# Optimization experiments

Hardware: AMD Instinct MI355X
Metric: run time of the kernel (lower is better)

The kernel has to match this reference:

```python
import jax, jax.numpy as jnp
import numpy as np

BATCH = 8
HEADS = 16
Q_LEN = 1024
K_LEN = 1024
HEAD_DIM = 64


def setup_inputs() -> dict:
    key = jax.random.key(0)
    kq, kk, kv, kl = jax.random.split(key, 4)
    queries = jax.random.normal(kq, (BATCH * HEADS, Q_LEN, HEAD_DIM), dtype=jnp.float32)
    keys = jax.random.normal(kk, (BATCH * HEADS, K_LEN, HEAD_DIM), dtype=jnp.float32)
    values = jax.random.normal(kv, (BATCH * HEADS, K_LEN, HEAD_DIM), dtype=jnp.float32)
    valid_lens = jax.random.randint(kl, (BATCH,), 0, K_LEN, dtype=jnp.int64)
    return {"queries": queries, "keys": keys, "values": values, "valid_lens": valid_lens}


def reference(queries, keys, values, valid_lens):
    # queries/keys/values: [B*H, S, d]; valid_lens: [B] int
    bh, q_len, d = queries.shape
    k_len = keys.shape[1]
    b = valid_lens.shape[0]
    h = bh // b
    scale = 1.0 / float(d) ** 0.5
    # [B*H, q, k] scores
    scores = jnp.einsum("bqd,bkd->bqk", queries, keys) * scale
    # encode_mask: True where key position >= valid_len -> fill with -1e6
    mask = jnp.arange(k_len)[None, :] >= valid_lens[:, None]  # [B, k]
    scores = scores.reshape(b, h, q_len, k_len)
    scores = jnp.where(mask[:, None, None, :], jnp.float32(-1000000.0), scores)
    attn = jax.nn.softmax(scores, axis=-1)  # [B, H, q, k]
    out = jnp.einsum("bhqk,bhkd->bhqd", attn, values.reshape(b, h, k_len, d))
    return out.reshape(bh, q_len, d)
```

## Files before the change

### kernel.cpp

```cpp
#include <hip/hip_runtime.h>


#define H_PER_B 16
#define QL 1024
#define KL 1024
#define DH 64
#define KT 64
#define QW 16
#define NW 8
#define QB (QW * NW)
#define KST 72
#define VST 72
#define PST 72

typedef float  f32x4  __attribute__((ext_vector_type(4)));
typedef short  bf16x8 __attribute__((ext_vector_type(8)));
typedef short  bf16x4 __attribute__((ext_vector_type(4)));

__device__ __forceinline__ short f2bf(float f) {
    unsigned u = __builtin_bit_cast(unsigned, f);
    u += 0x7FFFu + ((u >> 16) & 1u);
    return (short)(u >> 16);
}

__global__ __launch_bounds__(512) void attn_fwd(
    const float* __restrict__ Q, const float* __restrict__ K,
    const float* __restrict__ V, const int* __restrict__ vlen_p,
    float* __restrict__ O)
{
    const int qtile = blockIdx.x;
    const int bh    = blockIdx.y;
    const int vlen  = vlen_p[bh / H_PER_B];

    const int tid  = threadIdx.x;
    const int wave = tid >> 6;
    const int lane = tid & 63;
    const int lg   = lane >> 4;
    const int lr   = lane & 15;

    const float* Qb = Q + ((size_t)bh * QL + (size_t)qtile * QB + (size_t)wave * QW) * DH;
    const float* Kb = K + (size_t)bh * KL * DH;
    const float* Vb = V + (size_t)bh * KL * DH;

    __shared__ short Ks[KT][KST];
    __shared__ short VsT[DH][VST];
    __shared__ short Ps[NW][QW][PST];

    bf16x8 qf[2];
#pragma unroll
    for (int dc = 0; dc < 2; ++dc) {
        const float* p = Qb + (size_t)lr * DH + dc * 32 + 8 * lg;
        float4 a = *(const float4*)p;
        float4 b = *(const float4*)(p + 4);
        bf16x8 t;
        t[0]=f2bf(a.x); t[1]=f2bf(a.y); t[2]=f2bf(a.z); t[3]=f2bf(a.w);
        t[4]=f2bf(b.x); t[5]=f2bf(b.y); t[6]=f2bf(b.z); t[7]=f2bf(b.w);
        qf[dc] = t;
    }

    f32x4 acc[4];
#pragma unroll
    for (int i = 0; i < 4; ++i) acc[i] = (f32x4){0.f, 0.f, 0.f, 0.f};
    float lsum[4] = {0.f, 0.f, 0.f, 0.f};

    const bool all_masked = (vlen == 0);

    const int vd  = tid & 63;
    const int vk0 = (tid >> 6) * 8;
    const float* Vcol = Vb + vd;

    for (int kt0 = 0; kt0 < KL; kt0 += KT) {
        __syncthreads();

#pragma unroll
        for (int i = 0; i < 2; ++i) {
            int idx = tid + i * 512;
            int kr  = idx >> 4;
            int dc0 = (idx & 15) * 4;
            float4 kv = *(const float4*)(Kb + (size_t)(kt0 + kr) * DH + dc0);
            bf16x4 t;
            t[0]=f2bf(kv.x); t[1]=f2bf(kv.y); t[2]=f2bf(kv.z); t[3]=f2bf(kv.w);
            *(bf16x4*)&Ks[kr][dc0] = t;
        }

        {
            float v[8];
#pragma unroll
            for (int j = 0; j < 8; ++j)
                v[j] = Vcol[(size_t)(kt0 + vk0 + j) * DH];
            bf16x8 t;
#pragma unroll
            for (int j = 0; j < 8; ++j) t[j] = f2bf(v[j]);
            *(bf16x8*)&VsT[vd][vk0] = t;
        }
        __syncthreads();

        f32x4 s[4];
#pragma unroll
        for (int kh = 0; kh < 4; ++kh) {
            f32x4 c = (f32x4){0.f, 0.f, 0.f, 0.f};
#pragma unroll
            for (int dc = 0; dc < 2; ++dc) {
                bf16x8 kf = *(const bf16x8*)&Ks[kh * 16 + lr][dc * 32 + 8 * lg];
                c = __builtin_amdgcn_mfma_f32_16x16x32_bf16(qf[dc], kf, c, 0, 0, 0);
            }
            s[kh] = c;
        }

#pragma unroll
        for (int kh = 0; kh < 4; ++kh) {
            const int  kpos   = kt0 + kh * 16 + lr;
            const bool masked = (kpos >= vlen);
#pragma unroll
            for (int r = 0; r < 4; ++r) {
                float p;
                if (masked) p = all_masked ? 1.0f : 0.0f;
                else        p = __expf(s[kh][r] * 0.125f);
                lsum[r] += p;
                Ps[wave][lg * 4 + r][kh * 16 + lr] = f2bf(p);
            }
        }

#pragma unroll
        for (int u = 0; u < 2; ++u) {
            bf16x8 pf = *(const bf16x8*)&Ps[wave][lr][u * 32 + 8 * lg];
#pragma unroll
            for (int dt = 0; dt < 4; ++dt) {
                bf16x8 vf = *(const bf16x8*)&VsT[dt * 16 + lr][u * 32 + 8 * lg];
                acc[dt] = __builtin_amdgcn_mfma_f32_16x16x32_bf16(pf, vf, acc[dt], 0, 0, 0);
            }
        }
    }

    float inv[4];
#pragma unroll
    for (int r = 0; r < 4; ++r) {
        float sum = lsum[r];
#pragma unroll
        for (int off = 1; off < 16; off <<= 1)
            sum += __shfl_xor(sum, off, 64);
        inv[r] = 1.0f / sum;
    }

    float* Ob = O + ((size_t)bh * QL + (size_t)qtile * QB + (size_t)wave * QW) * DH;
#pragma unroll
    for (int r = 0; r < 4; ++r)
#pragma unroll
        for (int dt = 0; dt < 4; ++dt)
            Ob[(size_t)(lg * 4 + r) * DH + dt * 16 + lr] = acc[dt][r] * inv[r];
}

extern "C" void kernel_launch(void* const* d_in, const int* in_sizes, int n_in,
                              void* d_out, int out_size, void* d_ws, size_t ws_size,
                              hipStream_t stream) {
    (void)in_sizes; (void)n_in; (void)d_ws; (void)ws_size; (void)out_size;
    const float* Q    = (const float*)d_in[0];
    const float* K    = (const float*)d_in[1];
    const float* V    = (const float*)d_in[2];
    const int*   vlen = (const int*)d_in[3];
    float*       O    = (float*)d_out;

    dim3 grid(QL / QB, 128);
    dim3 block(512);
    attn_fwd<<<grid, block, 0, stream>>>(Q, K, V, vlen, O);
}
```

Baseline: 194.2 us.

## Skip fully masked key tiles and double-buffer K/V staging

```diff
diff --git a/kernel.cpp b/kernel.cpp
--- a/kernel.cpp
+++ b/kernel.cpp
@@ -11,16 +11,22 @@
 #define QB (QW * NW)
 #define KST 72
 #define VST 72
-#define PST 72
+#define PST 68
 
 typedef float  f32x4  __attribute__((ext_vector_type(4)));
 typedef short  bf16x8 __attribute__((ext_vector_type(8)));
 typedef short  bf16x4 __attribute__((ext_vector_type(4)));
 
-__device__ __forceinline__ short f2bf(float f) {
+__device__ __forceinline__ unsigned bfbits(float f) {
     unsigned u = __builtin_bit_cast(unsigned, f);
     u += 0x7FFFu + ((u >> 16) & 1u);
-    return (short)(u >> 16);
+    return u >> 16;
+}
+__device__ __forceinline__ unsigned pk2(float a, float b) {
+    return bfbits(a) | (bfbits(b) << 16);
+}
+__device__ __forceinline__ short s2bf(float f) {
+    return (short)bfbits(f);
 }
 
 __global__ __launch_bounds__(512) void attn_fwd(
@@ -28,8 +34,8 @@
     const float* __restrict__ V, const int* __restrict__ vlen_p,
     float* __restrict__ O)
 {
-    const int qtile = blockIdx.x;
-    const int bh    = blockIdx.y;
+    const int bh    = blockIdx.x;
+    const int qtile = blockIdx.y;
     const int vlen  = vlen_p[bh / H_PER_B];
 
     const int tid  = threadIdx.x;
@@ -42,20 +48,23 @@
     const float* Kb = K + (size_t)bh * KL * DH;
     const float* Vb = V + (size_t)bh * KL * DH;
 
-    __shared__ short Ks[KT][KST];
-    __shared__ short VsT[DH][VST];
-    __shared__ short Ps[NW][QW][PST];
+    __shared__ short Ks [2][KT][KST];
+    __shared__ short VsT[2][DH][VST];
+    __shared__ short Ps [NW][QW][PST];
 
+    const float QSCALE = 0.18033688011112042f;
     bf16x8 qf[2];
 #pragma unroll
     for (int dc = 0; dc < 2; ++dc) {
         const float* p = Qb + (size_t)lr * DH + dc * 32 + 8 * lg;
         float4 a = *(const float4*)p;
         float4 b = *(const float4*)(p + 4);
-        bf16x8 t;
-        t[0]=f2bf(a.x); t[1]=f2bf(a.y); t[2]=f2bf(a.z); t[3]=f2bf(a.w);
-        t[4]=f2bf(b.x); t[5]=f2bf(b.y); t[6]=f2bf(b.z); t[7]=f2bf(b.w);
-        qf[dc] = t;
+        uint4 u;
+        u.x = pk2(a.x * QSCALE, a.y * QSCALE);
+        u.y = pk2(a.z * QSCALE, a.w * QSCALE);
+        u.z = pk2(b.x * QSCALE, b.y * QSCALE);
+        u.w = pk2(b.z * QSCALE, b.w * QSCALE);
+        qf[dc] = __builtin_bit_cast(bf16x8, u);
     }
 
     f32x4 acc[4];
@@ -63,73 +72,83 @@
     for (int i = 0; i < 4; ++i) acc[i] = (f32x4){0.f, 0.f, 0.f, 0.f};
     float lsum[4] = {0.f, 0.f, 0.f, 0.f};
 
-    const bool all_masked = (vlen == 0);
+    const bool  all_masked = (vlen == 0);
+    const float msel       = all_masked ? 1.0f : 0.0f;
+    const int nt = all_masked ? (KL / KT) : ((vlen + KT - 1) >> 6);
 
+    const int kr0 = tid >> 4;
+    const int dc0 = (tid & 15) * 4;
     const int vd  = tid & 63;
     const int vk0 = (tid >> 6) * 8;
     const float* Vcol = Vb + vd;
 
-    for (int kt0 = 0; kt0 < KL; kt0 += KT) {
+    float4 ka[2];
+    float  va[8];
+
+#define LOADK(t)                                                              \
+    {                                                                         \
+        const float* kp = Kb + (size_t)((t) * KT) * DH;                       \
+        ka[0] = *(const float4*)(kp + (size_t)kr0 * DH + dc0);                \
+        ka[1] = *(const float4*)(kp + (size_t)(kr0 + 32) * DH + dc0);         \
+    }
+#define LOADV(t)                                                              \
+    _Pragma("unroll")                                                         \
+    for (int j = 0; j < 8; ++j)                                               \
+        va[j] = Vcol[(size_t)((t) * KT + vk0 + j) * DH];
+#define STOREKV(b)                                                            \
+    {                                                                         \
+        uint2 k0 = {pk2(ka[0].x, ka[0].y), pk2(ka[0].z, ka[0].w)};            \
+        uint2 k1 = {pk2(ka[1].x, ka[1].y), pk2(ka[1].z, ka[1].w)};            \
+        *(bf16x4*)&Ks[b][kr0][dc0]      = __builtin_bit_cast(bf16x4, k0);     \
+        *(bf16x4*)&Ks[b][kr0 + 32][dc0] = __builtin_bit_cast(bf16x4, k1);     \
+        uint4 vv = {pk2(va[0], va[1]), pk2(va[2], va[3]),                     \
+                    pk2(va[4], va[5]), pk2(va[6], va[7])};                    \
+        *(bf16x8*)&VsT[b][vd][vk0] = __builtin_bit_cast(bf16x8, vv);          \
+    }
+
+    LOADK(0); LOADV(0); STOREKV(0);
+
+    for (int t = 0; t < nt; ++t) {
+        const int buf = t & 1;
         __syncthreads();
 
-#pragma unroll
-        for (int i = 0; i < 2; ++i) {
-            int idx = tid + i * 512;
-            int kr  = idx >> 4;
-            int dc0 = (idx & 15) * 4;
-            float4 kv = *(const float4*)(Kb + (size_t)(kt0 + kr) * DH + dc0);
-            bf16x4 t;
-            t[0]=f2bf(kv.x); t[1]=f2bf(kv.y); t[2]=f2bf(kv.z); t[3]=f2bf(kv.w);
-            *(bf16x4*)&Ks[kr][dc0] = t;
-        }
+        if (t + 1 < nt) { LOADK(t + 1); LOADV(t + 1); }
+        const int kt0 = t * KT;
 
-        {
-            float v[8];
-#pragma unroll
-            for (int j = 0; j < 8; ++j)
-                v[j] = Vcol[(size_t)(kt0 + vk0 + j) * DH];
-            bf16x8 t;
-#pragma unroll
-            for (int j = 0; j < 8; ++j) t[j] = f2bf(v[j]);
-            *(bf16x8*)&VsT[vd][vk0] = t;
-        }
-        __syncthreads();
-
-        f32x4 s[4];
 #pragma unroll
         for (int kh = 0; kh < 4; ++kh) {
             f32x4 c = (f32x4){0.f, 0.f, 0.f, 0.f};
 #pragma unroll
             for (int dc = 0; dc < 2; ++dc) {
-                bf16x8 kf = *(const bf16x8*)&Ks[kh * 16 + lr][dc * 32 + 8 * lg];
+                bf16x8 kf = *(const bf16x8*)&Ks[buf][kh * 16 + lr][dc * 32 + 8 * lg];
                 c = __builtin_amdgcn_mfma_f32_16x16x32_bf16(qf[dc], kf, c, 0, 0, 0);
             }
-            s[kh] = c;
-        }
-
-#pragma unroll
-        for (int kh = 0; kh < 4; ++kh) {
             const int  kpos   = kt0 + kh * 16 + lr;
             const bool masked = (kpos >= vlen);
 #pragma unroll
             for (int r = 0; r < 4; ++r) {
-                float p;
-                if (masked) p = all_masked ? 1.0f : 0.0f;
-                else        p = __expf(s[kh][r] * 0.125f);
+                float e = __builtin_amdgcn_exp2f(c[r]);
+                float p = masked ? msel : e;
                 lsum[r] += p;
-                Ps[wave][lg * 4 + r][kh * 16 + lr] = f2bf(p);
+                Ps[wave][lg * 4 + r][kh * 16 + lr] = s2bf(p);
             }
         }
 
 #pragma unroll
         for (int u = 0; u < 2; ++u) {
-            bf16x8 pf = *(const bf16x8*)&Ps[wave][lr][u * 32 + 8 * lg];
+            bf16x4 plo = *(const bf16x4*)&Ps[wave][lr][u * 32 + 8 * lg];
+            bf16x4 phi = *(const bf16x4*)&Ps[wave][lr][u * 32 + 8 * lg + 4];
+            bf16x8 pf;
+#pragma unroll
+            for (int j = 0; j < 4; ++j) { pf[j] = plo[j]; pf[4 + j] = phi[j]; }
 #pragma unroll
             for (int dt = 0; dt < 4; ++dt) {
-                bf16x8 vf = *(const bf16x8*)&VsT[dt * 16 + lr][u * 32 + 8 * lg];
+                bf16x8 vf = *(const bf16x8*)&VsT[buf][dt * 16 + lr][u * 32 + 8 * lg];
                 acc[dt] = __builtin_amdgcn_mfma_f32_16x16x32_bf16(pf, vf, acc[dt], 0, 0, 0);
             }
         }
+
+        if (t + 1 < nt) STOREKV((t + 1) & 1);
     }
 
     float inv[4];
@@ -160,7 +179,7 @@
     const int*   vlen = (const int*)d_in[3];
     float*       O    = (float*)d_out;
 
-    dim3 grid(QL / QB, 128);
+    dim3 grid(128, QL / QB);
     dim3 block(512);
     attn_fwd<<<grid, block, 0, stream>>>(Q, K, V, vlen, O);
 }
```

Measured after the change: 168.5 us. 1.15x faster.
